# Optimization experiments

Hardware: AMD Instinct MI355X
Metric: run time of the kernel (lower is better)

The kernel has to match this reference:

```python
import jax, jax.numpy as jnp
import numpy as np

N, L, D, HEADS = 32, 128, 128, 4
B = 64
MHSA_RESIDUAL = False  # module default


def setup_inputs() -> dict:
    key = jax.random.key(0)
    ks = jax.random.split(key, 21)
    g = lambda k, shape, s=0.05: jax.random.normal(k, shape, dtype=jnp.float32) * s
    return {
        "X": jax.random.normal(ks[0], (B, L, N), dtype=jnp.float32),
        # per-variable encoder LSTM weights, stacked over N (torch gate order i,f,g,o)
        "enc_Wih": g(ks[1], (N, 4 * D)),        # input size is 1 -> (4d,1) squeezed
        "enc_Whh": g(ks[2], (N, 4 * D, D)),
        "enc_bih": g(ks[3], (N, 4 * D)),
        "enc_bhh": g(ks[4], (N, 4 * D)),
        "pool_w": g(ks[5], (N, D)),
        "pool_b": g(ks[6], (N,)),
        # nn.MultiheadAttention packed in-proj + out-proj
        "Wqkv": g(ks[7], (3 * D, D)),
        "bqkv": g(ks[8], (3 * D,)),
        "Wo": g(ks[9], (D, D)),
        "bo": g(ks[10], (D,)),
        # per-variable decoder: init_h/init_c Linear(d, d), LSTM, out Linear(d,1)
        "dec_ih_W": g(ks[11], (N, D, D)),
        "dec_ih_b": g(ks[12], (N, D)),
        "dec_ic_W": g(ks[13], (N, D, D)),
        "dec_ic_b": g(ks[14], (N, D)),
        "dec_Wih": g(ks[15], (N, 4 * D)),       # unused at runtime: decoder input is zeros
        "dec_Whh": g(ks[16], (N, 4 * D, D)),
        "dec_bih": g(ks[17], (N, 4 * D)),
        "dec_bhh": g(ks[18], (N, 4 * D)),
        "dec_out_W": g(ks[19], (N, D)),
        "dec_out_b": g(ks[20], (N,)),
    }


def _lstm_cell(pre, c):
    i, f, g, o = jnp.split(pre, 4, axis=-1)
    c_new = jax.nn.sigmoid(f) * c + jax.nn.sigmoid(i) * jnp.tanh(g)
    h_new = jax.nn.sigmoid(o) * jnp.tanh(c_new)
    return h_new, c_new


def reference(X, enc_Wih, enc_Whh, enc_bih, enc_bhh, pool_w, pool_b,
              Wqkv, bqkv, Wo, bo,
              dec_ih_W, dec_ih_b, dec_ic_W, dec_ic_b,
              dec_Wih, dec_Whh, dec_bih, dec_bhh, dec_out_W, dec_out_b):
    Bx = X.shape[0]
    # ---- N per-variable LSTM encoders, batched over the N axis ----
    x_enc = jnp.transpose(X[:, :L - 1, :], (1, 2, 0))  # (L-1, N, B)
    h0 = jnp.zeros((N, Bx, D), X.dtype)

    def enc_step(carry, x_t):
        h, c = carry
        pre = (x_t[..., None] * enc_Wih[:, None, :]
               + jnp.einsum('nbd,ngd->nbg', h, enc_Whh)
               + (enc_bih + enc_bhh)[:, None, :])
        h, c = _lstm_cell(pre, c)
        return (h, c), h

    _, H = jax.lax.scan(enc_step, (h0, h0), x_enc)  # (L-1, N, B, D)

    # temporal attention pooling (softmax over time)
    s = jnp.einsum('tnbd,nd->tnb', H, pool_w) + pool_b[None, :, None]
    a = jax.nn.softmax(s, axis=0)
    C = jnp.transpose(jnp.einsum('tnb,tnbd->nbd', a, H), (1, 0, 2))  # (B, N, D)

    # ---- MHSA over the variable axis ----
    qkv = C @ Wqkv.T + bqkv  # (B, N, 3D)
    q, k, v = jnp.split(qkv, 3, axis=-1)
    dh = D // HEADS
    split = lambda t: t.reshape(Bx, N, HEADS, dh).transpose(0, 2, 1, 3)  # (B,h,N,dh)
    q, k, v = split(q), split(k), split(v)
    attn = jax.nn.softmax(jnp.einsum('bhqd,bhkd->bhqk', q, k) / jnp.sqrt(jnp.float32(dh)), axis=-1)
    A = jnp.einsum('bhqk,bhkd->bhqd', attn, v).transpose(0, 2, 1, 3).reshape(Bx, N, D)
    A = A @ Wo.T + bo
    C_star = C + A if MHSA_RESIDUAL else A  # (B, N, D)

    # ---- N per-variable LSTM decoders, batched over the N axis ----
    cs = jnp.transpose(C_star, (1, 0, 2))  # (N, B, D)
    h = jnp.tanh(jnp.einsum('nbd,ned->nbe', cs, dec_ih_W) + dec_ih_b[:, None, :])
    c = jnp.tanh(jnp.einsum('nbd,ned->nbe', cs, dec_ic_W) + dec_ic_b[:, None, :])

    def dec_step(carry, _):
        h, c = carry
        # decoder input is identically zero -> W_ih contributes nothing
        pre = jnp.einsum('nbd,ngd->nbg', h, dec_Whh) + (dec_bih + dec_bhh)[:, None, :]
        h, c = _lstm_cell(pre, c)
        return (h, c), h

    _, Y = jax.lax.scan(dec_step, (h, c), None, length=L)  # (L, N, B, D)
    O = jnp.einsum('lnbd,nd->lnb', Y, dec_out_W) + dec_out_b[None, :, None]  # (L, N, B)
    recon = jnp.transpose(O[:L - 1], (2, 0, 1))  # (B, L-1, N)
    pred = O[L - 1].T                             # (B, N)
    return recon, pred, C_star
```

## Files before the change

kernel.cpp:

```cpp
#include <hip/hip_runtime.h>


typedef _Float16 h8  __attribute__((ext_vector_type(8)));
typedef _Float16 h4v __attribute__((ext_vector_type(4)));
typedef float    f4  __attribute__((ext_vector_type(4)));

#define DI __device__ __forceinline__

constexpr int NV  = 32;
constexpr int LT  = 128;
constexpr int DH  = 128;
constexpr int GG  = 4 * DH;
constexpr int BR  = 8;
constexpr int NW  = 8;
constexpr int TPB = NW * 64;
constexpr int HSTR = DH + 8;
constexpr float LOG2E = 1.4426950408889634f;

DI float rcp_(float x) { return __builtin_amdgcn_rcpf(x); }
DI float ex2_(float x) { return __builtin_amdgcn_exp2f(x); }

DI float tanh_(float x) {
    float xc = fminf(fmaxf(x, -20.0f), 20.0f);
    float E = ex2_(2.0f * LOG2E * xc);
    return (E - 1.0f) * rcp_(E + 1.0f);
}

DI float lstm_cell(float iv, float fv, float gv, float ov, float& c) {
    float Ai  = ex2_(-LOG2E * iv);
    float Bg  = ex2_(2.0f * LOG2E * gv);
    float sf  = rcp_(1.0f + ex2_(-LOG2E * fv));
    float itg = (Bg - 1.0f) * rcp_((1.0f + Ai) * (1.0f + Bg));
    c = fmaf(sf, c, itg);
    float cc = fminf(fmaxf(c, -20.0f), 20.0f);
    float Ec = ex2_(2.0f * LOG2E * cc);
    float Eo = ex2_(-LOG2E * ov);
    return (Ec - 1.0f) * rcp_((1.0f + Eo) * (1.0f + Ec));
}

DI h8 cvt8(f4 a, f4 b) {
    h8 r;
    r[0] = (_Float16)a[0]; r[1] = (_Float16)a[1];
    r[2] = (_Float16)a[2]; r[3] = (_Float16)a[3];
    r[4] = (_Float16)b[0]; r[5] = (_Float16)b[1];
    r[6] = (_Float16)b[2]; r[7] = (_Float16)b[3];
    return r;
}

__global__ __launch_bounds__(TPB, 2)
void enc_kernel(const float* __restrict__ X,
                const float* __restrict__ Wih,
                const float* __restrict__ Whh,
                const float* __restrict__ bih,
                const float* __restrict__ bhh,
                const float* __restrict__ poolw,
                float* __restrict__ Cout)
{
    const int n    = blockIdx.x >> 3;
    const int b0   = (blockIdx.x & 7) * BR;
    const int tid  = threadIdx.x;
    const int wv   = tid >> 6;
    const int lane = tid & 63;
    const int quad = lane >> 4;
    const int l16  = lane & 15;
    const int dmy  = wv * 16 + l16;

    __shared__ _Float16 hbuf[2][16 * HSTR];
    __shared__ float xs[(LT - 1) * BR];
    __shared__ float pfin[2][BR];

    h8 Wf[4][4];
    float wihr[4], biasr[4];
#pragma unroll
    for (int g4 = 0; g4 < 4; ++g4) {
        const int g = g4 * DH + dmy;
        const float* wrow = Whh + (size_t)(n * GG + g) * DH;
#pragma unroll
        for (int kc = 0; kc < 4; ++kc) {
            f4 w0 = *(const f4*)(wrow + kc * 32 + quad * 8);
            f4 w1 = *(const f4*)(wrow + kc * 32 + quad * 8 + 4);
            Wf[g4][kc] = cvt8(w0, w1);
        }
        wihr[g4]  = Wih[n * GG + g];
        biasr[g4] = bih[n * GG + g] + bhh[n * GG + g];
    }
    h8 Bp[4];
#pragma unroll
    for (int kc = 0; kc < 4; ++kc) {
        if (l16 == 0) {
            f4 p0 = *(const f4*)(poolw + n * DH + kc * 32 + quad * 8);
            f4 p1 = *(const f4*)(poolw + n * DH + kc * 32 + quad * 8 + 4);
            Bp[kc] = cvt8(p0, p1);
        } else {
            Bp[kc] = (h8)(_Float16)0.0f;
        }
    }

    for (int i = tid; i < (LT - 1) * BR; i += TPB)
        xs[i] = X[((size_t)(b0 + (i & 7)) * LT + (i >> 3)) * NV + n];
    for (int i = tid; i < 2 * 16 * HSTR; i += TPB)
        ((_Float16*)hbuf)[i] = (_Float16)0.0f;
    __syncthreads();

    float cst[2]   = {0.f, 0.f};
    float lsum[2]  = {0.f, 0.f};
    float acc[2]   = {0.f, 0.f};
    float hprev[2] = {0.f, 0.f};

    for (int t = 0; t < LT - 1; ++t) {
        const _Float16* hb = hbuf[t & 1];
        h8 a[4];
#pragma unroll
        for (int kc = 0; kc < 4; ++kc)
            a[kc] = *(const h8*)(hb + l16 * HSTR + kc * 32 + quad * 8);

        f4 pre[4];
#pragma unroll
        for (int g4 = 0; g4 < 4; ++g4) {
            f4 bsp = {biasr[g4], biasr[g4], biasr[g4], biasr[g4]};
            pre[g4] = bsp;
        }
#pragma unroll
        for (int kc = 0; kc < 4; ++kc)
#pragma unroll
            for (int g4 = 0; g4 < 4; ++g4)
                pre[g4] = __builtin_amdgcn_mfma_f32_16x16x32_f16(
                    a[kc], Wf[g4][kc], pre[g4], 0, 0, 0);

        if (wv == 0) {
            f4 sp = {0.f, 0.f, 0.f, 0.f};
#pragma unroll
            for (int kc = 0; kc < 4; ++kc)
                sp = __builtin_amdgcn_mfma_f32_16x16x32_f16(a[kc], Bp[kc], sp, 0, 0, 0);
            if (l16 == 0) {
                pfin[t & 1][quad * 2 + 0] = ex2_(LOG2E * sp[0]);
                pfin[t & 1][quad * 2 + 1] = ex2_(LOG2E * sp[1]);
            }
        }

        float hv[2];
#pragma unroll
        for (int r = 0; r < 2; ++r) {
            const float xb = xs[t * BR + quad * 2 + r];
            hv[r] = lstm_cell(pre[0][r] + xb * wihr[0],
                              pre[1][r] + xb * wihr[1],
                              pre[2][r] + xb * wihr[2],
                              pre[3][r] + xb * wihr[3], cst[r]);
        }

        _Float16* hn = hbuf[(t + 1) & 1];
#pragma unroll
        for (int r = 0; r < 2; ++r)
            hn[(quad * 4 + r) * HSTR + dmy] = (_Float16)hv[r];
        __syncthreads();

        if (t > 0) {
#pragma unroll
            for (int r = 0; r < 2; ++r) {
                const float p = pfin[t & 1][quad * 2 + r];
                lsum[r] += p;
                acc[r] = fmaf(p, hprev[r], acc[r]);
            }
        }
#pragma unroll
        for (int r = 0; r < 2; ++r) hprev[r] = hv[r];
    }

    if (wv == 0) {
        const _Float16* hb = hbuf[(LT - 1) & 1];
        h8 a[4];
#pragma unroll
        for (int kc = 0; kc < 4; ++kc)
            a[kc] = *(const h8*)(hb + l16 * HSTR + kc * 32 + quad * 8);
        f4 sp = {0.f, 0.f, 0.f, 0.f};
#pragma unroll
        for (int kc = 0; kc < 4; ++kc)
            sp = __builtin_amdgcn_mfma_f32_16x16x32_f16(a[kc], Bp[kc], sp, 0, 0, 0);
        if (l16 == 0) {
            pfin[(LT - 1) & 1][quad * 2 + 0] = ex2_(LOG2E * sp[0]);
            pfin[(LT - 1) & 1][quad * 2 + 1] = ex2_(LOG2E * sp[1]);
        }
    }
    __syncthreads();
#pragma unroll
    for (int r = 0; r < 2; ++r) {
        const float p = pfin[(LT - 1) & 1][quad * 2 + r];
        lsum[r] += p;
        acc[r] = fmaf(p, hprev[r], acc[r]);
    }

#pragma unroll
    for (int r = 0; r < 2; ++r) {
        const int b = b0 + quad * 2 + r;
        Cout[((size_t)b * NV + n) * DH + dmy] = acc[r] * rcp_(lsum[r]);
    }
}

constexpr int CS2 = DH + 8;
constexpr int QS  = 40;

__global__ __launch_bounds__(256)
void attn_kernel(const float* __restrict__ Cin,
                 const float* __restrict__ Wqkv,
                 const float* __restrict__ bqkv,
                 float* __restrict__ Astage)
{
    const int b    = blockIdx.x >> 2;
    const int hh   = blockIdx.x & 3;
    const int tid  = threadIdx.x;
    const int wv   = tid >> 6;
    const int lane = tid & 63;
    const int quad = lane >> 4;
    const int l16  = lane & 15;

    __shared__ _Float16 Cb[NV][CS2];
    __shared__ _Float16 qs[NV][QS], ks[NV][QS], vT[NV][QS];
    __shared__ float    S[NV][NV + 1];
    __shared__ _Float16 P[NV][QS];

    for (int i = tid; i < NV * DH / 4; i += 256) {
        const int nn = i >> 5, d4 = (i & 31) * 4;
        f4 v = *(const f4*)(Cin + ((size_t)b * NV + nn) * DH + d4);
        h4v hv4;
        hv4[0] = (_Float16)v[0]; hv4[1] = (_Float16)v[1];
        hv4[2] = (_Float16)v[2]; hv4[3] = (_Float16)v[3];
        *(h4v*)(&Cb[nn][d4]) = hv4;
    }
    __syncthreads();

    const int m0 = (wv >> 1) * 16;
    const int n0 = (wv & 1) * 16;

    h8 a[4];
#pragma unroll
    for (int kc = 0; kc < 4; ++kc)
        a[kc] = *(const h8*)(&Cb[m0 + l16][kc * 32 + quad * 8]);

#pragma unroll
    for (int mat = 0; mat < 3; ++mat) {
        const int rbase = mat * DH + hh * 32;
        const float* wrow = Wqkv + (size_t)(rbase + n0 + l16) * DH;
        const float bias  = bqkv[rbase + n0 + l16];
        f4 acc = {bias, bias, bias, bias};
#pragma unroll
        for (int kc = 0; kc < 4; ++kc) {
            f4 w0 = *(const f4*)(wrow + kc * 32 + quad * 8);
            f4 w1 = *(const f4*)(wrow + kc * 32 + quad * 8 + 4);
            acc = __builtin_amdgcn_mfma_f32_16x16x32_f16(a[kc], cvt8(w0, w1), acc, 0, 0, 0);
        }
#pragma unroll
        for (int r = 0; r < 4; ++r) {
            const int tok = m0 + quad * 4 + r, col = n0 + l16;
            if (mat == 0)      qs[tok][col] = (_Float16)acc[r];
            else if (mat == 1) ks[tok][col] = (_Float16)acc[r];
            else               vT[col][tok] = (_Float16)acc[r];
        }
    }
    __syncthreads();

    {
        h8 aq = *(const h8*)(&qs[m0 + l16][quad * 8]);
        h8 bk = *(const h8*)(&ks[n0 + l16][quad * 8]);
        f4 sc = {0.f, 0.f, 0.f, 0.f};
        sc = __builtin_amdgcn_mfma_f32_16x16x32_f16(aq, bk, sc, 0, 0, 0);
#pragma unroll
        for (int r = 0; r < 4; ++r)
            S[m0 + quad * 4 + r][n0 + l16] = sc[r] * 0.17677669529663687f;
    }
    __syncthreads();

    if (tid < NV) {
        float mx = -1e30f;
        for (int j = 0; j < NV; ++j) mx = fmaxf(mx, S[tid][j]);
        float l = 0.0f;
        float p[NV];
#pragma unroll
        for (int j = 0; j < NV; ++j) {
            p[j] = ex2_(LOG2E * (S[tid][j] - mx));
            l += p[j];
        }
        const float rl = rcp_(l);
#pragma unroll
        for (int j = 0; j < NV; ++j) P[tid][j] = (_Float16)(p[j] * rl);
    }
    __syncthreads();

    {
        h8 ap = *(const h8*)(&P[m0 + l16][quad * 8]);
        h8 bv = *(const h8*)(&vT[n0 + l16][quad * 8]);
        f4 av = {0.f, 0.f, 0.f, 0.f};
        av = __builtin_amdgcn_mfma_f32_16x16x32_f16(ap, bv, av, 0, 0, 0);
#pragma unroll
        for (int r = 0; r < 4; ++r) {
            const int tok = m0 + quad * 4 + r;
            Astage[((size_t)b * NV + tok) * DH + hh * 32 + n0 + l16] = av[r];
        }
    }
}

__global__ __launch_bounds__(256)
void outproj_kernel(const float* __restrict__ Wo,
                    const float* __restrict__ bo,
                    float* __restrict__ AC)
{
    const int mb   = blockIdx.x * 16;
    const int tid  = threadIdx.x;
    const int wv   = tid >> 6;
    const int lane = tid & 63;
    const int quad = lane >> 4;
    const int l16  = lane & 15;

    __shared__ _Float16 As[16][HSTR];

    for (int i = tid; i < 16 * DH / 4; i += 256) {
        const int rr = i >> 5, d4 = (i & 31) * 4;
        f4 v = *(const f4*)(AC + ((size_t)(mb + rr)) * DH + d4);
        h4v hv4;
        hv4[0] = (_Float16)v[0]; hv4[1] = (_Float16)v[1];
        hv4[2] = (_Float16)v[2]; hv4[3] = (_Float16)v[3];
        *(h4v*)(&As[rr][d4]) = hv4;
    }
    __syncthreads();

    h8 a[4];
#pragma unroll
    for (int kc = 0; kc < 4; ++kc)
        a[kc] = *(const h8*)(&As[l16][kc * 32 + quad * 8]);

#pragma unroll
    for (int i = 0; i < 2; ++i) {
        const int n0 = (wv * 2 + i) * 16;
        const float* wrow = Wo + (size_t)(n0 + l16) * DH;
        const float bias  = bo[n0 + l16];
        f4 acc = {bias, bias, bias, bias};
#pragma unroll
        for (int kc = 0; kc < 4; ++kc) {
            f4 w0 = *(const f4*)(wrow + kc * 32 + quad * 8);
            f4 w1 = *(const f4*)(wrow + kc * 32 + quad * 8 + 4);
            acc = __builtin_amdgcn_mfma_f32_16x16x32_f16(a[kc], cvt8(w0, w1), acc, 0, 0, 0);
        }
#pragma unroll
        for (int r = 0; r < 4; ++r)
            AC[((size_t)(mb + quad * 4 + r)) * DH + n0 + l16] = acc[r];
    }
}

__global__ __launch_bounds__(TPB, 2)
void dec_kernel(const float* __restrict__ Cstar,
                const float* __restrict__ ihW,
                const float* __restrict__ ihb,
                const float* __restrict__ icW,
                const float* __restrict__ icb,
                const float* __restrict__ Whh,
                const float* __restrict__ bih,
                const float* __restrict__ bhh,
                const float* __restrict__ outW,
                const float* __restrict__ outb,
                float* __restrict__ recon,
                float* __restrict__ pred)
{
    const int n    = blockIdx.x >> 3;
    const int b0   = (blockIdx.x & 7) * BR;
    const int tid  = threadIdx.x;
    const int wv   = tid >> 6;
    const int lane = tid & 63;
    const int quad = lane >> 4;
    const int l16  = lane & 15;
    const int dmy  = wv * 16 + l16;

    __shared__ _Float16 hbuf[2][16 * HSTR];

    h8 Wf[4][4];
    float biasr[4];
#pragma unroll
    for (int g4 = 0; g4 < 4; ++g4) {
        const int g = g4 * DH + dmy;
        const float* wrow = Whh + (size_t)(n * GG + g) * DH;
#pragma unroll
        for (int kc = 0; kc < 4; ++kc) {
            f4 w0 = *(const f4*)(wrow + kc * 32 + quad * 8);
            f4 w1 = *(const f4*)(wrow + kc * 32 + quad * 8 + 4);
            Wf[g4][kc] = cvt8(w0, w1);
        }
        biasr[g4] = bih[n * GG + g] + bhh[n * GG + g];
    }
    h8 Bo[4];
#pragma unroll
    for (int kc = 0; kc < 4; ++kc) {
        if (l16 == 0) {
            f4 p0 = *(const f4*)(outW + n * DH + kc * 32 + quad * 8);
            f4 p1 = *(const f4*)(outW + n * DH + kc * 32 + quad * 8 + 4);
            Bo[kc] = cvt8(p0, p1);
        } else {
            Bo[kc] = (h8)(_Float16)0.0f;
        }
    }
    const float ob = outb[n];

    for (int i = tid; i < 2 * 16 * HSTR; i += TPB)
        ((_Float16*)hbuf)[i] = (_Float16)0.0f;
    __syncthreads();
    if (tid < 256) {
        const int j = tid >> 5, d4 = (tid & 31) * 4;
        const int row = (j >> 1) * 4 + (j & 1);
        f4 v = *(const f4*)(Cstar + ((size_t)(b0 + j) * NV + n) * DH + d4);
        h4v hv4;
        hv4[0] = (_Float16)v[0]; hv4[1] = (_Float16)v[1];
        hv4[2] = (_Float16)v[2]; hv4[3] = (_Float16)v[3];
        *(h4v*)(&hbuf[0][row * HSTR + d4]) = hv4;
    }
    __syncthreads();

    float cst[2], hv0[2];
    {
        h8 a[4];
#pragma unroll
        for (int kc = 0; kc < 4; ++kc)
            a[kc] = *(const h8*)(hbuf[0] + l16 * HSTR + kc * 32 + quad * 8);
        const float bh = ihb[n * DH + dmy];
        const float bc = icb[n * DH + dmy];
        f4 Ph = {bh, bh, bh, bh};
        f4 Pc = {bc, bc, bc, bc};
        const float* hrow = ihW + (size_t)(n * DH + dmy) * DH;
        const float* crow = icW + (size_t)(n * DH + dmy) * DH;
#pragma unroll
        for (int kc = 0; kc < 4; ++kc) {
            f4 w0 = *(const f4*)(hrow + kc * 32 + quad * 8);
            f4 w1 = *(const f4*)(hrow + kc * 32 + quad * 8 + 4);
            Ph = __builtin_amdgcn_mfma_f32_16x16x32_f16(a[kc], cvt8(w0, w1), Ph, 0, 0, 0);
            f4 u0 = *(const f4*)(crow + kc * 32 + quad * 8);
            f4 u1 = *(const f4*)(crow + kc * 32 + quad * 8 + 4);
            Pc = __builtin_amdgcn_mfma_f32_16x16x32_f16(a[kc], cvt8(u0, u1), Pc, 0, 0, 0);
        }
#pragma unroll
        for (int r = 0; r < 2; ++r) {
            hv0[r] = tanh_(Ph[r]);
            cst[r] = tanh_(Pc[r]);
        }
    }
    __syncthreads();
#pragma unroll
    for (int r = 0; r < 2; ++r)
        hbuf[0][(quad * 4 + r) * HSTR + dmy] = (_Float16)hv0[r];
    __syncthreads();

    for (int t = 0; t < LT; ++t) {
        const _Float16* hb = hbuf[t & 1];
        h8 a[4];
#pragma unroll
        for (int kc = 0; kc < 4; ++kc)
            a[kc] = *(const h8*)(hb + l16 * HSTR + kc * 32 + quad * 8);

        f4 pre[4];
#pragma unroll
        for (int g4 = 0; g4 < 4; ++g4) {
            f4 bsp = {biasr[g4], biasr[g4], biasr[g4], biasr[g4]};
            pre[g4] = bsp;
        }
#pragma unroll
        for (int kc = 0; kc < 4; ++kc)
#pragma unroll
            for (int g4 = 0; g4 < 4; ++g4)
                pre[g4] = __builtin_amdgcn_mfma_f32_16x16x32_f16(
                    a[kc], Wf[g4][kc], pre[g4], 0, 0, 0);

        if (wv == 0 && t > 0) {
            f4 so = {0.f, 0.f, 0.f, 0.f};
#pragma unroll
            for (int kc = 0; kc < 4; ++kc)
                so = __builtin_amdgcn_mfma_f32_16x16x32_f16(a[kc], Bo[kc], so, 0, 0, 0);
            if (l16 == 0) {
#pragma unroll
                for (int r = 0; r < 2; ++r) {
                    const int b = b0 + quad * 2 + r;
                    recon[((size_t)b * (LT - 1) + (t - 1)) * NV + n] = so[r] + ob;
                }
            }
        }

        float hv[2];
#pragma unroll
        for (int r = 0; r < 2; ++r)
            hv[r] = lstm_cell(pre[0][r], pre[1][r], pre[2][r], pre[3][r], cst[r]);

        _Float16* hn = hbuf[(t + 1) & 1];
#pragma unroll
        for (int r = 0; r < 2; ++r)
            hn[(quad * 4 + r) * HSTR + dmy] = (_Float16)hv[r];
        __syncthreads();
    }

    if (wv == 0) {
        const _Float16* hb = hbuf[LT & 1];
        h8 a[4];
#pragma unroll
        for (int kc = 0; kc < 4; ++kc)
            a[kc] = *(const h8*)(hb + l16 * HSTR + kc * 32 + quad * 8);
        f4 so = {0.f, 0.f, 0.f, 0.f};
#pragma unroll
        for (int kc = 0; kc < 4; ++kc)
            so = __builtin_amdgcn_mfma_f32_16x16x32_f16(a[kc], Bo[kc], so, 0, 0, 0);
        if (l16 == 0) {
#pragma unroll
            for (int r = 0; r < 2; ++r) {
                const int b = b0 + quad * 2 + r;
                pred[(size_t)b * NV + n] = so[r] + ob;
            }
        }
    }
}

extern "C" void kernel_launch(void* const* d_in, const int* in_sizes, int n_in,
                              void* d_out, int out_size, void* d_ws, size_t ws_size,
                              hipStream_t stream) {
    (void)in_sizes; (void)n_in; (void)d_ws; (void)ws_size; (void)out_size;

    const float* X     = (const float*)d_in[0];
    const float* eWih  = (const float*)d_in[1];
    const float* eWhh  = (const float*)d_in[2];
    const float* ebih  = (const float*)d_in[3];
    const float* ebhh  = (const float*)d_in[4];
    const float* poolw = (const float*)d_in[5];
    const float* Wqkv  = (const float*)d_in[7];
    const float* bqkv  = (const float*)d_in[8];
    const float* Wo    = (const float*)d_in[9];
    const float* bo    = (const float*)d_in[10];
    const float* dihW  = (const float*)d_in[11];
    const float* dihb  = (const float*)d_in[12];
    const float* dicW  = (const float*)d_in[13];
    const float* dicb  = (const float*)d_in[14];
    const float* dWhh  = (const float*)d_in[16];
    const float* dbih  = (const float*)d_in[17];
    const float* dbhh  = (const float*)d_in[18];
    const float* doutW = (const float*)d_in[19];
    const float* doutb = (const float*)d_in[20];

    float* out   = (float*)d_out;
    float* recon = out;
    float* pred  = out + 64 * 127 * 32;
    float* Cstar = out + 64 * 127 * 32 + 64 * 32;
    float* Cpool = out;

    enc_kernel<<<dim3(256), dim3(TPB), 0, stream>>>(
        X, eWih, eWhh, ebih, ebhh, poolw, Cpool);
    attn_kernel<<<dim3(256), dim3(256), 0, stream>>>(
        Cpool, Wqkv, bqkv, Cstar);
    outproj_kernel<<<dim3(128), dim3(256), 0, stream>>>(
        Wo, bo, Cstar);
    dec_kernel<<<dim3(256), dim3(TPB), 0, stream>>>(
        Cstar, dihW, dihb, dicW, dicb, dWhh, dbih, dbhh,
        doutW, doutb, recon, pred);
}
```

Before: 293.1 us.

## Halve batch rows per block to launch 512 recurrent LSTM blocks

Cuts the batch rows per block in the encoder and decoder LSTM kernels from 8 to 4 and doubles the grid to 512 blocks, ordering blocks variable-fastest. This is meant to spread the serial recurrences over more compute units and shorten each block's per-step epilogue work. The decoder also gathers its reconstruction outputs in shared memory and writes them out in one pass after the loop, replacing scattered per-step global stores. In exchange, each MFMA tile now uses only one of its 16 rows per quad-group, so MFMA work per useful row doubles, and the recurrent weights are loaded by twice as many blocks.

```diff
diff --git a/kernel.cpp b/kernel.cpp
--- a/kernel.cpp
+++ b/kernel.cpp
@@ -11,7 +11,7 @@
 constexpr int LT  = 128;
 constexpr int DH  = 128;
 constexpr int GG  = 4 * DH;
-constexpr int BR  = 8;
+constexpr int BR  = 4;
 constexpr int NW  = 8;
 constexpr int TPB = NW * 64;
 constexpr int HSTR = DH + 8;
@@ -56,8 +56,8 @@
                 const float* __restrict__ poolw,
                 float* __restrict__ Cout)
 {
-    const int n    = blockIdx.x >> 3;
-    const int b0   = (blockIdx.x & 7) * BR;
+    const int n    = blockIdx.x & 31;
+    const int b0   = (blockIdx.x >> 5) * BR;
     const int tid  = threadIdx.x;
     const int wv   = tid >> 6;
     const int lane = tid & 63;
@@ -97,15 +97,12 @@
     }
 
     for (int i = tid; i < (LT - 1) * BR; i += TPB)
-        xs[i] = X[((size_t)(b0 + (i & 7)) * LT + (i >> 3)) * NV + n];
+        xs[i] = X[((size_t)(b0 + (i & 3)) * LT + (i >> 2)) * NV + n];
     for (int i = tid; i < 2 * 16 * HSTR; i += TPB)
         ((_Float16*)hbuf)[i] = (_Float16)0.0f;
     __syncthreads();
 
-    float cst[2]   = {0.f, 0.f};
-    float lsum[2]  = {0.f, 0.f};
-    float acc[2]   = {0.f, 0.f};
-    float hprev[2] = {0.f, 0.f};
+    float cst = 0.f, lsum = 0.f, acc = 0.f, hprev = 0.f;
 
     for (int t = 0; t < LT - 1; ++t) {
         const _Float16* hb = hbuf[t & 1];
@@ -132,38 +129,24 @@
 #pragma unroll
             for (int kc = 0; kc < 4; ++kc)
                 sp = __builtin_amdgcn_mfma_f32_16x16x32_f16(a[kc], Bp[kc], sp, 0, 0, 0);
-            if (l16 == 0) {
-                pfin[t & 1][quad * 2 + 0] = ex2_(LOG2E * sp[0]);
-                pfin[t & 1][quad * 2 + 1] = ex2_(LOG2E * sp[1]);
-            }
-        }
-
-        float hv[2];
-#pragma unroll
-        for (int r = 0; r < 2; ++r) {
-            const float xb = xs[t * BR + quad * 2 + r];
-            hv[r] = lstm_cell(pre[0][r] + xb * wihr[0],
-                              pre[1][r] + xb * wihr[1],
-                              pre[2][r] + xb * wihr[2],
-                              pre[3][r] + xb * wihr[3], cst[r]);
-        }
-
-        _Float16* hn = hbuf[(t + 1) & 1];
-#pragma unroll
-        for (int r = 0; r < 2; ++r)
-            hn[(quad * 4 + r) * HSTR + dmy] = (_Float16)hv[r];
+            if (l16 == 0) pfin[t & 1][quad] = ex2_(LOG2E * sp[0]);
+        }
+
+        const float xb = xs[t * BR + quad];
+        const float hv = lstm_cell(pre[0][0] + xb * wihr[0],
+                                   pre[1][0] + xb * wihr[1],
+                                   pre[2][0] + xb * wihr[2],
+                                   pre[3][0] + xb * wihr[3], cst);
+
+        hbuf[(t + 1) & 1][(quad * 4) * HSTR + dmy] = (_Float16)hv;
         __syncthreads();
 
         if (t > 0) {
-#pragma unroll
-            for (int r = 0; r < 2; ++r) {
-                const float p = pfin[t & 1][quad * 2 + r];
-                lsum[r] += p;
-                acc[r] = fmaf(p, hprev[r], acc[r]);
-            }
-        }
-#pragma unroll
-        for (int r = 0; r < 2; ++r) hprev[r] = hv[r];
+            const float p = pfin[t & 1][quad];
+            lsum += p;
+            acc = fmaf(p, hprev, acc);
+        }
+        hprev = hv;
     }
 
     if (wv == 0) {
@@ -176,24 +159,15 @@
 #pragma unroll
         for (int kc = 0; kc < 4; ++kc)
             sp = __builtin_amdgcn_mfma_f32_16x16x32_f16(a[kc], Bp[kc], sp, 0, 0, 0);
-        if (l16 == 0) {
-            pfin[(LT - 1) & 1][quad * 2 + 0] = ex2_(LOG2E * sp[0]);
-            pfin[(LT - 1) & 1][quad * 2 + 1] = ex2_(LOG2E * sp[1]);
-        }
-    }
-    __syncthreads();
-#pragma unroll
-    for (int r = 0; r < 2; ++r) {
-        const float p = pfin[(LT - 1) & 1][quad * 2 + r];
-        lsum[r] += p;
-        acc[r] = fmaf(p, hprev[r], acc[r]);
-    }
-
-#pragma unroll
-    for (int r = 0; r < 2; ++r) {
-        const int b = b0 + quad * 2 + r;
-        Cout[((size_t)b * NV + n) * DH + dmy] = acc[r] * rcp_(lsum[r]);
-    }
+        if (l16 == 0) pfin[(LT - 1) & 1][quad] = ex2_(LOG2E * sp[0]);
+    }
+    __syncthreads();
+    {
+        const float p = pfin[(LT - 1) & 1][quad];
+        lsum += p;
+        acc = fmaf(p, hprev, acc);
+    }
+    Cout[((size_t)(b0 + quad) * NV + n) * DH + dmy] = acc * rcp_(lsum);
 }
 
 constexpr int CS2 = DH + 8;
@@ -359,8 +333,8 @@
                 float* __restrict__ recon,
                 float* __restrict__ pred)
 {
-    const int n    = blockIdx.x >> 3;
-    const int b0   = (blockIdx.x & 7) * BR;
+    const int n    = blockIdx.x & 31;
+    const int b0   = (blockIdx.x >> 5) * BR;
     const int tid  = threadIdx.x;
     const int wv   = tid >> 6;
     const int lane = tid & 63;
@@ -369,6 +343,7 @@
     const int dmy  = wv * 16 + l16;
 
     __shared__ _Float16 hbuf[2][16 * HSTR];
+    __shared__ float obuf[LT - 1][BR];
 
     h8 Wf[4][4];
     float biasr[4];
@@ -400,18 +375,17 @@
     for (int i = tid; i < 2 * 16 * HSTR; i += TPB)
         ((_Float16*)hbuf)[i] = (_Float16)0.0f;
     __syncthreads();
-    if (tid < 256) {
+    if (tid < 128) {
         const int j = tid >> 5, d4 = (tid & 31) * 4;
-        const int row = (j >> 1) * 4 + (j & 1);
         f4 v = *(const f4*)(Cstar + ((size_t)(b0 + j) * NV + n) * DH + d4);
         h4v hv4;
         hv4[0] = (_Float16)v[0]; hv4[1] = (_Float16)v[1];
         hv4[2] = (_Float16)v[2]; hv4[3] = (_Float16)v[3];
-        *(h4v*)(&hbuf[0][row * HSTR + d4]) = hv4;
-    }
-    __syncthreads();
-
-    float cst[2], hv0[2];
+        *(h4v*)(&hbuf[0][(j * 4) * HSTR + d4]) = hv4;
+    }
+    __syncthreads();
+
+    float cst, hv0;
     {
         h8 a[4];
 #pragma unroll
@@ -432,16 +406,11 @@
             f4 u1 = *(const f4*)(crow + kc * 32 + quad * 8 + 4);
             Pc = __builtin_amdgcn_mfma_f32_16x16x32_f16(a[kc], cvt8(u0, u1), Pc, 0, 0, 0);
         }
-#pragma unroll
-        for (int r = 0; r < 2; ++r) {
-            hv0[r] = tanh_(Ph[r]);
-            cst[r] = tanh_(Pc[r]);
-        }
-    }
-    __syncthreads();
-#pragma unroll
-    for (int r = 0; r < 2; ++r)
-        hbuf[0][(quad * 4 + r) * HSTR + dmy] = (_Float16)hv0[r];
+        hv0 = tanh_(Ph[0]);
+        cst = tanh_(Pc[0]);
+    }
+    __syncthreads();
+    hbuf[0][(quad * 4) * HSTR + dmy] = (_Float16)hv0;
     __syncthreads();
 
     for (int t = 0; t < LT; ++t) {
@@ -469,24 +438,12 @@
 #pragma unroll
             for (int kc = 0; kc < 4; ++kc)
                 so = __builtin_amdgcn_mfma_f32_16x16x32_f16(a[kc], Bo[kc], so, 0, 0, 0);
-            if (l16 == 0) {
-#pragma unroll
-                for (int r = 0; r < 2; ++r) {
-                    const int b = b0 + quad * 2 + r;
-                    recon[((size_t)b * (LT - 1) + (t - 1)) * NV + n] = so[r] + ob;
-                }
-            }
-        }
-
-        float hv[2];
-#pragma unroll
-        for (int r = 0; r < 2; ++r)
-            hv[r] = lstm_cell(pre[0][r], pre[1][r], pre[2][r], pre[3][r], cst[r]);
-
-        _Float16* hn = hbuf[(t + 1) & 1];
-#pragma unroll
-        for (int r = 0; r < 2; ++r)
-            hn[(quad * 4 + r) * HSTR + dmy] = (_Float16)hv[r];
+            if (l16 == 0) obuf[t - 1][quad] = so[0] + ob;
+        }
+
+        const float hv = lstm_cell(pre[0][0], pre[1][0], pre[2][0], pre[3][0], cst);
+
+        hbuf[(t + 1) & 1][(quad * 4) * HSTR + dmy] = (_Float16)hv;
         __syncthreads();
     }
 
@@ -500,13 +457,13 @@
 #pragma unroll
         for (int kc = 0; kc < 4; ++kc)
             so = __builtin_amdgcn_mfma_f32_16x16x32_f16(a[kc], Bo[kc], so, 0, 0, 0);
-        if (l16 == 0) {
-#pragma unroll
-            for (int r = 0; r < 2; ++r) {
-                const int b = b0 + quad * 2 + r;
-                pred[(size_t)b * NV + n] = so[r] + ob;
-            }
-        }
+        if (l16 == 0) pred[(size_t)(b0 + quad) * NV + n] = so[0] + ob;
+    }
+
+    if (tid < LT - 1) {
+#pragma unroll
+        for (int b = 0; b < BR; ++b)
+            recon[((size_t)(b0 + b) * (LT - 1) + tid) * NV + n] = obuf[tid][b];
     }
 }
 
@@ -541,13 +498,13 @@
     float* Cstar = out + 64 * 127 * 32 + 64 * 32;
     float* Cpool = out;
 
-    enc_kernel<<<dim3(256), dim3(TPB), 0, stream>>>(
+    enc_kernel<<<dim3(512), dim3(TPB), 0, stream>>>(
         X, eWih, eWhh, ebih, ebhh, poolw, Cpool);
     attn_kernel<<<dim3(256), dim3(256), 0, stream>>>(
         Cpool, Wqkv, bqkv, Cstar);
     outproj_kernel<<<dim3(128), dim3(256), 0, stream>>>(
         Wo, bo, Cstar);
-    dec_kernel<<<dim3(256), dim3(TPB), 0, stream>>>(
+    dec_kernel<<<dim3(512), dim3(TPB), 0, stream>>>(
         Cstar, dihW, dihb, dicW, dicb, dWhh, dbih, dbhh,
         doutW, doutb, recon, pred);
 }
```

Result: slower. 407.2 us (+38.9%).

## Fold gate exp2 scales into weights, seed MFMA with bias, buffer decoder outputs

Applied to the files above, without the earlier changes.

The -log2e and 2*log2e scale factors for the gate activations are folded into the fp16 recurrent weights, the input weights and the biases at load time, so the per-step LSTM cell needs fewer multiplies. The cell now computes the new c with a single reciprocal. The bias is passed as the accumulator of the first MFMA, and the decoder stages recon outputs in shared memory so they can be written once after the loop. The block-to-(n, batch) mapping is also swapped. Scaling the weights before the fp16 conversion slightly changes rounding, and c is computed through a combined fraction that may lose some precision.

```diff
diff --git a/kernel.cpp b/kernel.cpp
--- a/kernel.cpp
+++ b/kernel.cpp
@@ -4,6 +4,7 @@
 typedef _Float16 h8  __attribute__((ext_vector_type(8)));
 typedef _Float16 h4v __attribute__((ext_vector_type(4)));
 typedef float    f4  __attribute__((ext_vector_type(4)));
+typedef float    f2v __attribute__((ext_vector_type(2)));
 
 #define DI __device__ __forceinline__
 
@@ -27,14 +28,16 @@
 }
 
 DI float lstm_cell(float iv, float fv, float gv, float ov, float& c) {
-    float Ai  = ex2_(-LOG2E * iv);
-    float Bg  = ex2_(2.0f * LOG2E * gv);
-    float sf  = rcp_(1.0f + ex2_(-LOG2E * fv));
-    float itg = (Bg - 1.0f) * rcp_((1.0f + Ai) * (1.0f + Bg));
-    c = fmaf(sf, c, itg);
+    float Ai = ex2_(iv);
+    float Af = ex2_(fv);
+    float Bg = ex2_(gv);
+    float ai1 = 1.0f + Ai, af1 = 1.0f + Af, bg1 = 1.0f + Bg;
+    float P = ai1 * bg1;
+    float N = fmaf(c, P, (Bg - 1.0f) * af1);
+    c = N * rcp_(P * af1);
     float cc = fminf(fmaxf(c, -20.0f), 20.0f);
     float Ec = ex2_(2.0f * LOG2E * cc);
-    float Eo = ex2_(-LOG2E * ov);
+    float Eo = ex2_(ov);
     return (Ec - 1.0f) * rcp_((1.0f + Eo) * (1.0f + Ec));
 }
 
@@ -46,6 +49,16 @@
     r[6] = (_Float16)b[2]; r[7] = (_Float16)b[3];
     return r;
 }
+DI h8 cvt8s(f4 a, f4 b, float s) {
+    h8 r;
+    r[0] = (_Float16)(a[0] * s); r[1] = (_Float16)(a[1] * s);
+    r[2] = (_Float16)(a[2] * s); r[3] = (_Float16)(a[3] * s);
+    r[4] = (_Float16)(b[0] * s); r[5] = (_Float16)(b[1] * s);
+    r[6] = (_Float16)(b[2] * s); r[7] = (_Float16)(b[3] * s);
+    return r;
+}
+
+__constant__ float GSC[4] = {-LOG2E, -LOG2E, 2.0f * LOG2E, -LOG2E};
 
 __global__ __launch_bounds__(TPB, 2)
 void enc_kernel(const float* __restrict__ X,
@@ -56,8 +69,8 @@
                 const float* __restrict__ poolw,
                 float* __restrict__ Cout)
 {
-    const int n    = blockIdx.x >> 3;
-    const int b0   = (blockIdx.x & 7) * BR;
+    const int n    = blockIdx.x & 31;
+    const int b0   = (blockIdx.x >> 5) * BR;
     const int tid  = threadIdx.x;
     const int wv   = tid >> 6;
     const int lane = tid & 63;
@@ -70,19 +83,22 @@
     __shared__ float pfin[2][BR];
 
     h8 Wf[4][4];
-    float wihr[4], biasr[4];
+    float wihr[4];
+    f4 bsp[4];
 #pragma unroll
     for (int g4 = 0; g4 < 4; ++g4) {
+        const float s = GSC[g4];
         const int g = g4 * DH + dmy;
         const float* wrow = Whh + (size_t)(n * GG + g) * DH;
 #pragma unroll
         for (int kc = 0; kc < 4; ++kc) {
             f4 w0 = *(const f4*)(wrow + kc * 32 + quad * 8);
             f4 w1 = *(const f4*)(wrow + kc * 32 + quad * 8 + 4);
-            Wf[g4][kc] = cvt8(w0, w1);
-        }
-        wihr[g4]  = Wih[n * GG + g];
-        biasr[g4] = bih[n * GG + g] + bhh[n * GG + g];
+            Wf[g4][kc] = cvt8s(w0, w1, s);
+        }
+        wihr[g4] = Wih[n * GG + g] * s;
+        const float bb = (bih[n * GG + g] + bhh[n * GG + g]) * s;
+        bsp[g4] = (f4){bb, bb, bb, bb};
     }
     h8 Bp[4];
 #pragma unroll
@@ -90,7 +106,7 @@
         if (l16 == 0) {
             f4 p0 = *(const f4*)(poolw + n * DH + kc * 32 + quad * 8);
             f4 p1 = *(const f4*)(poolw + n * DH + kc * 32 + quad * 8 + 4);
-            Bp[kc] = cvt8(p0, p1);
+            Bp[kc] = cvt8s(p0, p1, LOG2E);
         } else {
             Bp[kc] = (h8)(_Float16)0.0f;
         }
@@ -116,12 +132,11 @@
 
         f4 pre[4];
 #pragma unroll
-        for (int g4 = 0; g4 < 4; ++g4) {
-            f4 bsp = {biasr[g4], biasr[g4], biasr[g4], biasr[g4]};
-            pre[g4] = bsp;
-        }
-#pragma unroll
-        for (int kc = 0; kc < 4; ++kc)
+        for (int g4 = 0; g4 < 4; ++g4)
+            pre[g4] = __builtin_amdgcn_mfma_f32_16x16x32_f16(
+                a[0], Wf[g4][0], bsp[g4], 0, 0, 0);
+#pragma unroll
+        for (int kc = 1; kc < 4; ++kc)
 #pragma unroll
             for (int g4 = 0; g4 < 4; ++g4)
                 pre[g4] = __builtin_amdgcn_mfma_f32_16x16x32_f16(
@@ -133,19 +148,19 @@
             for (int kc = 0; kc < 4; ++kc)
                 sp = __builtin_amdgcn_mfma_f32_16x16x32_f16(a[kc], Bp[kc], sp, 0, 0, 0);
             if (l16 == 0) {
-                pfin[t & 1][quad * 2 + 0] = ex2_(LOG2E * sp[0]);
-                pfin[t & 1][quad * 2 + 1] = ex2_(LOG2E * sp[1]);
+                pfin[t & 1][quad * 2 + 0] = ex2_(sp[0]);
+                pfin[t & 1][quad * 2 + 1] = ex2_(sp[1]);
             }
         }
 
+        const f2v xv = *(const f2v*)(xs + t * BR + quad * 2);
         float hv[2];
 #pragma unroll
         for (int r = 0; r < 2; ++r) {
-            const float xb = xs[t * BR + quad * 2 + r];
-            hv[r] = lstm_cell(pre[0][r] + xb * wihr[0],
-                              pre[1][r] + xb * wihr[1],
-                              pre[2][r] + xb * wihr[2],
-                              pre[3][r] + xb * wihr[3], cst[r]);
+            hv[r] = lstm_cell(fmaf(xv[r], wihr[0], pre[0][r]),
+                              fmaf(xv[r], wihr[1], pre[1][r]),
+                              fmaf(xv[r], wihr[2], pre[2][r]),
+                              fmaf(xv[r], wihr[3], pre[3][r]), cst[r]);
         }
 
         _Float16* hn = hbuf[(t + 1) & 1];
@@ -177,8 +192,8 @@
         for (int kc = 0; kc < 4; ++kc)
             sp = __builtin_amdgcn_mfma_f32_16x16x32_f16(a[kc], Bp[kc], sp, 0, 0, 0);
         if (l16 == 0) {
-            pfin[(LT - 1) & 1][quad * 2 + 0] = ex2_(LOG2E * sp[0]);
-            pfin[(LT - 1) & 1][quad * 2 + 1] = ex2_(LOG2E * sp[1]);
+            pfin[(LT - 1) & 1][quad * 2 + 0] = ex2_(sp[0]);
+            pfin[(LT - 1) & 1][quad * 2 + 1] = ex2_(sp[1]);
         }
     }
     __syncthreads();
@@ -188,7 +203,6 @@
         lsum[r] += p;
         acc[r] = fmaf(p, hprev[r], acc[r]);
     }
-
 #pragma unroll
     for (int r = 0; r < 2; ++r) {
         const int b = b0 + quad * 2 + r;
@@ -359,8 +373,8 @@
                 float* __restrict__ recon,
                 float* __restrict__ pred)
 {
-    const int n    = blockIdx.x >> 3;
-    const int b0   = (blockIdx.x & 7) * BR;
+    const int n    = blockIdx.x & 31;
+    const int b0   = (blockIdx.x >> 5) * BR;
     const int tid  = threadIdx.x;
     const int wv   = tid >> 6;
     const int lane = tid & 63;
@@ -369,20 +383,23 @@
     const int dmy  = wv * 16 + l16;
 
     __shared__ _Float16 hbuf[2][16 * HSTR];
+    __shared__ float obuf[LT - 1][BR];
 
     h8 Wf[4][4];
-    float biasr[4];
+    f4 bsp[4];
 #pragma unroll
     for (int g4 = 0; g4 < 4; ++g4) {
+        const float s = GSC[g4];
         const int g = g4 * DH + dmy;
         const float* wrow = Whh + (size_t)(n * GG + g) * DH;
 #pragma unroll
         for (int kc = 0; kc < 4; ++kc) {
             f4 w0 = *(const f4*)(wrow + kc * 32 + quad * 8);
             f4 w1 = *(const f4*)(wrow + kc * 32 + quad * 8 + 4);
-            Wf[g4][kc] = cvt8(w0, w1);
-        }
-        biasr[g4] = bih[n * GG + g] + bhh[n * GG + g];
+            Wf[g4][kc] = cvt8s(w0, w1, s);
+        }
+        const float bb = (bih[n * GG + g] + bhh[n * GG + g]) * s;
+        bsp[g4] = (f4){bb, bb, bb, bb};
     }
     h8 Bo[4];
 #pragma unroll
@@ -453,12 +470,11 @@
 
         f4 pre[4];
 #pragma unroll
-        for (int g4 = 0; g4 < 4; ++g4) {
-            f4 bsp = {biasr[g4], biasr[g4], biasr[g4], biasr[g4]};
-            pre[g4] = bsp;
-        }
-#pragma unroll
-        for (int kc = 0; kc < 4; ++kc)
+        for (int g4 = 0; g4 < 4; ++g4)
+            pre[g4] = __builtin_amdgcn_mfma_f32_16x16x32_f16(
+                a[0], Wf[g4][0], bsp[g4], 0, 0, 0);
+#pragma unroll
+        for (int kc = 1; kc < 4; ++kc)
 #pragma unroll
             for (int g4 = 0; g4 < 4; ++g4)
                 pre[g4] = __builtin_amdgcn_mfma_f32_16x16x32_f16(
@@ -470,11 +486,8 @@
             for (int kc = 0; kc < 4; ++kc)
                 so = __builtin_amdgcn_mfma_f32_16x16x32_f16(a[kc], Bo[kc], so, 0, 0, 0);
             if (l16 == 0) {
-#pragma unroll
-                for (int r = 0; r < 2; ++r) {
-                    const int b = b0 + quad * 2 + r;
-                    recon[((size_t)b * (LT - 1) + (t - 1)) * NV + n] = so[r] + ob;
-                }
+                obuf[t - 1][quad * 2 + 0] = so[0] + ob;
+                obuf[t - 1][quad * 2 + 1] = so[1] + ob;
             }
         }
 
@@ -501,12 +514,15 @@
         for (int kc = 0; kc < 4; ++kc)
             so = __builtin_amdgcn_mfma_f32_16x16x32_f16(a[kc], Bo[kc], so, 0, 0, 0);
         if (l16 == 0) {
-#pragma unroll
-            for (int r = 0; r < 2; ++r) {
-                const int b = b0 + quad * 2 + r;
-                pred[(size_t)b * NV + n] = so[r] + ob;
-            }
-        }
+            pred[(size_t)(b0 + quad * 2 + 0) * NV + n] = so[0] + ob;
+            pred[(size_t)(b0 + quad * 2 + 1) * NV + n] = so[1] + ob;
+        }
+    }
+
+    if (tid < LT - 1) {
+#pragma unroll
+        for (int b = 0; b < BR; ++b)
+            recon[((size_t)(b0 + b) * (LT - 1) + tid) * NV + n] = obuf[tid][b];
     }
 }
 
```

Measured after the change: 292.8 us. Within noise of the previous version (-0.1%).
